# Optimization experiments

Measured on AMD Instinct MI355X. Metric: run time of the kernel, lower is better.

Reference implementation:

```python
import jax, jax.numpy as jnp
import numpy as np

B, C, H, W = 4, 512, 64, 64
CI = C // 4  # inner dim of q/k/v projections


def setup_inputs() -> dict:
    key = jax.random.key(0)
    ks = jax.random.split(key, 9)
    s = 1.0 / np.sqrt(C)
    si = 1.0 / np.sqrt(CI)
    return {
        "x": jax.random.normal(ks[0], (B, C, H, W), dtype=jnp.float32),
        "wq": jax.random.uniform(ks[1], (CI, C), jnp.float32, -s, s),
        "bq": jax.random.uniform(ks[2], (CI,), jnp.float32, -s, s),
        "wk": jax.random.uniform(ks[3], (CI, C), jnp.float32, -s, s),
        "bk": jax.random.uniform(ks[4], (CI,), jnp.float32, -s, s),
        "wv": jax.random.uniform(ks[5], (CI, C), jnp.float32, -s, s),
        "bv": jax.random.uniform(ks[6], (CI,), jnp.float32, -s, s),
        "wo": jax.random.uniform(ks[7], (C, CI), jnp.float32, -si, si),
        "bo": jax.random.uniform(ks[8], (C,), jnp.float32, -si, si),
    }


def reference(x, wq, bq, wk, bk, wv, bv, wo, bo):
    b, c, h, w = x.shape
    n = h * w
    xf = x.reshape(b, c, n)  # [B,C,N]
    # 1x1 convs == channel matmuls
    q = jnp.einsum('oc,bcn->bon', wq, xf) + bq[:, None]  # [B,CI,N]
    k = jnp.einsum('oc,bcn->bon', wk, xf) + bk[:, None]
    v = jnp.einsum('oc,bcn->bon', wv, xf) + bv[:, None]
    # energy[b,i,j] = sum_c q[b,c,i]*k[b,c,j]  (no scaling, per original)
    energy = jnp.einsum('bci,bcj->bij', q, k)  # [B,N,N]
    attn = jax.nn.softmax(energy, axis=-1)
    # out[b,c,i] = sum_j v[b,c,j] * attn[b,i,j]
    out = jnp.einsum('bcj,bij->bci', v, attn)  # [B,CI,N]
    out = jnp.einsum('oc,bcn->bon', wo, out) + bo[:, None]  # [B,C,N]
    out = out.reshape(b, c, h, w) + x
    return out
```

## Files before the change

### kernel.cpp

```cpp
#include <hip/hip_runtime.h>

#define N_TOK 4096
#define C_DIM 512
#define CI_DIM 128
#define B_DIM 4
#define KVSPLIT 4
#define KVBLK 32
#define NIT (N_TOK / KVSPLIT / KVBLK)
#define RESCALE_THR 8.0f

typedef unsigned short u16;
typedef unsigned int u32;
typedef unsigned long long u64;
typedef __attribute__((ext_vector_type(8))) short bf16x8;
typedef __attribute__((ext_vector_type(4))) float f32x4;
typedef __attribute__((ext_vector_type(8))) unsigned short u16x8;
typedef __attribute__((ext_vector_type(4))) float float4v;

typedef unsigned long long __attribute__((may_alias)) u64a;
typedef bf16x8 __attribute__((may_alias)) bf16x8a;
typedef u16x8 __attribute__((may_alias)) u16x8a;

__device__ __forceinline__ u16 f2bf(float f) {
    union { float f; u32 u; } v; v.f = f;
    u32 r = (v.u + 0x7fffu + ((v.u >> 16) & 1u)) >> 16;
    return (u16)r;
}
__device__ __forceinline__ float bf2f(u16 h) {
    union { u32 u; float f; } v; v.u = (u32)h << 16;
    return v.f;
}
__device__ __forceinline__ u32 cvt_pk_bf16(float a, float b) {
    u32 r;
    asm("v_cvt_pk_bf16_f32 %0, %1, %2" : "=v"(r) : "v"(a), "v"(b));
    return r;
}

__global__ __launch_bounds__(256) void xpose_kernel(
    const float* __restrict__ x, u16* __restrict__ xT)
{
    const int n0 = blockIdx.x * 64;
    const int c0 = blockIdx.y * 64;
    const int b  = blockIdx.z;
    __shared__ u16 Ts[64][72];
    const int t = threadIdx.x;

    const float* xb = x + (size_t)b * C_DIM * N_TOK;
    for (int idx = t; idx < 4096; idx += 256) {
        int c = idx >> 6, n = idx & 63;
        Ts[n][c] = f2bf(xb[(size_t)(c0 + c) * N_TOK + n0 + n]);
    }
    __syncthreads();
    u16* xTb = xT + (size_t)b * N_TOK * C_DIM;
    for (int idx = t; idx < 512; idx += 256) {
        int n = idx >> 3, c8 = idx & 7;
        *(u16x8*)&xTb[(size_t)(n0 + n) * C_DIM + c0 + c8 * 8] =
            *(u16x8*)&Ts[n][c8 * 8];
    }
}

__global__ __launch_bounds__(256) void wconv_kernel(
    const float* __restrict__ wq, const float* __restrict__ wk,
    const float* __restrict__ wv, const float* __restrict__ wo,
    u16* __restrict__ wqB, u16* __restrict__ wkB,
    u16* __restrict__ wvB, u16* __restrict__ woB)
{
    const int z = blockIdx.y;
    const float* src = (z == 0) ? wq : (z == 1) ? wk : (z == 2) ? wv : wo;
    u16* dst = (z == 0) ? wqB : (z == 1) ? wkB : (z == 2) ? wvB : woB;
    const int i0 = (blockIdx.x * 256 + threadIdx.x) * 8;
    float4v a = *(const float4v*)&src[i0];
    float4v b = *(const float4v*)&src[i0 + 4];
    u16x8 o;
    o[0] = f2bf(a[0]); o[1] = f2bf(a[1]); o[2] = f2bf(a[2]); o[3] = f2bf(a[3]);
    o[4] = f2bf(b[0]); o[5] = f2bf(b[1]); o[6] = f2bf(b[2]); o[7] = f2bf(b[3]);
    *(u16x8*)&dst[i0] = o;
}

__global__ __launch_bounds__(256) void qkv_gemm_kernel(
    const u16* __restrict__ xT,
    const u16* __restrict__ wqB, const u16* __restrict__ wkB,
    const u16* __restrict__ wvB,
    const float* __restrict__ bq, const float* __restrict__ bk,
    const float* __restrict__ bv,
    u16* __restrict__ qT, u16* __restrict__ kT, u16* __restrict__ vB)
{
    const int n0 = blockIdx.x * 128;
    const int b  = blockIdx.y;
    const int z  = blockIdx.z;
    const u16* wz = (z == 0) ? wqB : (z == 1) ? wkB : wvB;
    const float* bias = (z == 0) ? bq : (z == 1) ? bk : bv;

    __shared__ u16 Xs[128][72];
    __shared__ u16 Ws[128][72];

    const int t  = threadIdx.x;
    const int w  = t >> 6;
    const int l  = t & 63;
    const int lg = l >> 4;
    const int li = l & 15;
    const int cb = w * 32;

    const u16* xTb = xT + (size_t)b * N_TOK * C_DIM;

    const int srow = t >> 1;
    const int sh   = (t & 1) * 32;

    f32x4 acc[8][2];
#pragma unroll
    for (int m = 0; m < 8; ++m)
#pragma unroll
        for (int j = 0; j < 2; ++j)
#pragma unroll
            for (int r = 0; r < 4; ++r) acc[m][j][r] = 0.f;

    u16x8 xv[4], wv[4];
#pragma unroll
    for (int g = 0; g < 4; ++g) {
        xv[g] = *(const u16x8a*)&xTb[(size_t)(n0 + srow) * C_DIM + sh + g * 8];
        wv[g] = *(const u16x8a*)&wz[(size_t)srow * C_DIM + sh + g * 8];
    }

    const u16 (*A_lds)[72] = (z < 2) ? Xs : Ws;
    const u16 (*B_lds)[72] = (z < 2) ? Ws : Xs;

#pragma unroll 1
    for (int kk = 0; kk < C_DIM / 64; ++kk) {
        __syncthreads();
#pragma unroll
        for (int g = 0; g < 4; ++g) {
            *(u16x8a*)&Xs[srow][sh + g * 8] = xv[g];
            *(u16x8a*)&Ws[srow][sh + g * 8] = wv[g];
        }
        __syncthreads();

        if (kk + 1 < C_DIM / 64) {
            const int k0 = (kk + 1) * 64;
#pragma unroll
            for (int g = 0; g < 4; ++g) {
                xv[g] = *(const u16x8a*)&xTb[(size_t)(n0 + srow) * C_DIM + k0 + sh + g * 8];
                wv[g] = *(const u16x8a*)&wz[(size_t)srow * C_DIM + k0 + sh + g * 8];
            }
        }

#pragma unroll
        for (int kc = 0; kc < 2; ++kc) {
            bf16x8 af[8], bfv[2];
#pragma unroll
            for (int m = 0; m < 8; ++m)
                af[m] = *(const bf16x8a*)&A_lds[m * 16 + li][kc * 32 + lg * 8];
#pragma unroll
            for (int j = 0; j < 2; ++j)
                bfv[j] = *(const bf16x8a*)&B_lds[cb + j * 16 + li][kc * 32 + lg * 8];
            __builtin_amdgcn_s_setprio(1);
#pragma unroll
            for (int m = 0; m < 8; ++m)
#pragma unroll
                for (int j = 0; j < 2; ++j)
                    acc[m][j] = __builtin_amdgcn_mfma_f32_16x16x32_bf16(
                        af[m], bfv[j], acc[m][j], 0, 0, 0);
            __builtin_amdgcn_s_setprio(0);
        }
    }

    if (z < 2) {
        u16* dst = ((z == 0) ? qT : kT) + (size_t)b * N_TOK * CI_DIM;
#pragma unroll
        for (int j = 0; j < 2; ++j) {
            float bia = bias[cb + j * 16 + li];
#pragma unroll
            for (int m = 0; m < 8; ++m)
#pragma unroll
                for (int r = 0; r < 4; ++r)
                    dst[(size_t)(n0 + m * 16 + lg * 4 + r) * CI_DIM + cb + j * 16 + li] =
                        f2bf(acc[m][j][r] + bia);
        }
    } else {
        u16* dst = vB + (size_t)b * CI_DIM * N_TOK;
#pragma unroll
        for (int m = 0; m < 8; ++m)
#pragma unroll
            for (int r = 0; r < 4; ++r) {
                int o = m * 16 + lg * 4 + r;
                float bia = bias[o];
#pragma unroll
                for (int j = 0; j < 2; ++j)
                    dst[(size_t)o * N_TOK + n0 + cb + j * 16 + li] =
                        f2bf(acc[m][j][r] + bia);
            }
    }
}

__global__ __launch_bounds__(256) void attn_mfma_kernel(
    const u16* __restrict__ qT,
    const u16* __restrict__ kT,
    const u16* __restrict__ vB,
    u16* __restrict__ Opart,
    float* __restrict__ Mout,
    float* __restrict__ Lout)
{
    const int x   = blockIdx.x;
    const int qb  = x >> 4;
    const int b   = x & 3;
    const int kvh = (x >> 2) & 3;
    const int j_beg = kvh * (N_TOK / KVSPLIT);

    __shared__ u16 Ks[KVBLK][152];
    __shared__ u16 Vs[CI_DIM][56];
    __shared__ u16 Ps[4][32][40];

    const int t  = threadIdx.x;
    const int w  = t >> 6;
    const int l  = t & 63;
    const int lg = l >> 4;
    const int li = l & 15;
    const int qw = qb * 128 + w * 32;

    const int krow = t >> 3, kc8 = t & 7;
    const int vch  = t >> 1, vh  = t & 1;

    const u16* qTb = qT + (size_t)b * N_TOK * CI_DIM;
    const u16* kTb = kT + (size_t)b * N_TOK * CI_DIM;
    const u16* vBb = vB + (size_t)b * CI_DIM * N_TOK;

    bf16x8 qf[2][4];
#pragma unroll
    for (int qt = 0; qt < 2; ++qt)
#pragma unroll
        for (int kc = 0; kc < 4; ++kc)
            qf[qt][kc] = *(const bf16x8*)&qTb[(size_t)(qw + qt * 16 + li) * CI_DIM + kc * 32 + lg * 8];

    f32x4 Oacc[2][8];
#pragma unroll
    for (int qt = 0; qt < 2; ++qt)
#pragma unroll
        for (int ct = 0; ct < 8; ++ct)
#pragma unroll
            for (int r = 0; r < 4; ++r) Oacc[qt][ct][r] = 0.f;

    float mrun[2] = {-1e30f, -1e30f};
    float lrun[2] = {0.f, 0.f};

    u16x8 kv0, kv1, vv0, vv1;
    {
        const u16* ksrc = &kTb[(size_t)(j_beg + krow) * CI_DIM + kc8 * 16];
        kv0 = *(const u16x8a*)&ksrc[0];
        kv1 = *(const u16x8a*)&ksrc[8];
        const u16* vsrc = &vBb[(size_t)vch * N_TOK + j_beg + vh * 16];
        vv0 = *(const u16x8a*)&vsrc[0];
        vv1 = *(const u16x8a*)&vsrc[8];
    }

#pragma unroll 1
    for (int it = 0; it < NIT; ++it) {
        __syncthreads();
        *(u16x8a*)&Ks[krow][kc8 * 16]     = kv0;
        *(u16x8a*)&Ks[krow][kc8 * 16 + 8] = kv1;
        *(u16x8a*)&Vs[vch][vh * 16]       = vv0;
        *(u16x8a*)&Vs[vch][vh * 16 + 8]   = vv1;
        __syncthreads();

        if (it + 1 < NIT) {
            const int jn = j_beg + (it + 1) * KVBLK;
            const u16* ksrc = &kTb[(size_t)(jn + krow) * CI_DIM + kc8 * 16];
            kv0 = *(const u16x8a*)&ksrc[0];
            kv1 = *(const u16x8a*)&ksrc[8];
            const u16* vsrc = &vBb[(size_t)vch * N_TOK + jn + vh * 16];
            vv0 = *(const u16x8a*)&vsrc[0];
            vv1 = *(const u16x8a*)&vsrc[8];
        }

        bf16x8 ak[2][4];
#pragma unroll
        for (int jt = 0; jt < 2; ++jt)
#pragma unroll
            for (int kc = 0; kc < 4; ++kc)
                ak[jt][kc] = *(const bf16x8a*)&Ks[jt * 16 + li][kc * 32 + lg * 8];

        f32x4 sacc[2][2];
#pragma unroll
        for (int qt = 0; qt < 2; ++qt)
#pragma unroll
            for (int jt = 0; jt < 2; ++jt)
#pragma unroll
                for (int r = 0; r < 4; ++r) sacc[qt][jt][r] = 0.f;
        __builtin_amdgcn_s_setprio(1);
#pragma unroll
        for (int jt = 0; jt < 2; ++jt)
#pragma unroll
            for (int kc = 0; kc < 4; ++kc) {
                sacc[0][jt] = __builtin_amdgcn_mfma_f32_16x16x32_bf16(ak[jt][kc], qf[0][kc], sacc[0][jt], 0, 0, 0);
                sacc[1][jt] = __builtin_amdgcn_mfma_f32_16x16x32_bf16(ak[jt][kc], qf[1][kc], sacc[1][jt], 0, 0, 0);
            }
        __builtin_amdgcn_s_setprio(0);

#pragma unroll
        for (int qt = 0; qt < 2; ++qt) {
            float tl = sacc[qt][0][0];
#pragma unroll
            for (int jt = 0; jt < 2; ++jt)
#pragma unroll
                for (int r = 0; r < 4; ++r) tl = fmaxf(tl, sacc[qt][jt][r]);

            if (__any(tl > mrun[qt] + RESCALE_THR)) {
                float tmax = fmaxf(tl, __shfl_xor(tl, 16));
                tmax = fmaxf(tmax, __shfl_xor(tmax, 32));
                float mold = mrun[qt];
                float mnew = fmaxf(mold, tmax);
                float scale = __expf(mold - mnew);
                lrun[qt] *= scale;
                mrun[qt] = mnew;
#pragma unroll
                for (int r = 0; r < 4; ++r) {
                    float sc_r = __shfl(scale, lg * 4 + r);
#pragma unroll
                    for (int ct = 0; ct < 8; ++ct) Oacc[qt][ct][r] *= sc_r;
                }
            }
            float m = mrun[qt];
            float psum = 0.f;
#pragma unroll
            for (int jt = 0; jt < 2; ++jt) {
                float p0 = __expf(sacc[qt][jt][0] - m);
                float p1 = __expf(sacc[qt][jt][1] - m);
                float p2 = __expf(sacc[qt][jt][2] - m);
                float p3 = __expf(sacc[qt][jt][3] - m);
                psum += (p0 + p1) + (p2 + p3);
                u32 lo = cvt_pk_bf16(p0, p1);
                u32 hi = cvt_pk_bf16(p2, p3);
                u64 pk = (u64)lo | ((u64)hi << 32);
                *(u64a*)&Ps[w][qt * 16 + li][jt * 16 + lg * 4] = pk;
            }
            lrun[qt] += psum;
        }

        asm volatile("" ::: "memory");

        bf16x8 ap0 = *(const bf16x8a*)&Ps[w][li][lg * 8];
        bf16x8 ap1 = *(const bf16x8a*)&Ps[w][16 + li][lg * 8];
        __builtin_amdgcn_s_setprio(1);
#pragma unroll
        for (int ct = 0; ct < 8; ++ct) {
            bf16x8 bv = *(const bf16x8a*)&Vs[ct * 16 + li][lg * 8];
            Oacc[0][ct] = __builtin_amdgcn_mfma_f32_16x16x32_bf16(ap0, bv, Oacc[0][ct], 0, 0, 0);
            Oacc[1][ct] = __builtin_amdgcn_mfma_f32_16x16x32_bf16(ap1, bv, Oacc[1][ct], 0, 0, 0);
        }
        __builtin_amdgcn_s_setprio(0);
    }

#pragma unroll
    for (int qt = 0; qt < 2; ++qt) {
        lrun[qt] += __shfl_xor(lrun[qt], 16);
        lrun[qt] += __shfl_xor(lrun[qt], 32);
    }
    const size_t mlbase = ((size_t)kvh * B_DIM + b) * N_TOK + qw;
    if (lg == 0) {
#pragma unroll
        for (int qt = 0; qt < 2; ++qt) {
            Mout[mlbase + qt * 16 + li] = mrun[qt];
            Lout[mlbase + qt * 16 + li] = lrun[qt];
        }
    }
    u16* Ob = Opart + mlbase * CI_DIM;
#pragma unroll
    for (int qt = 0; qt < 2; ++qt)
#pragma unroll
        for (int ct = 0; ct < 8; ++ct)
#pragma unroll
            for (int r = 0; r < 4; ++r)
                Ob[(size_t)(qt * 16 + lg * 4 + r) * CI_DIM + ct * 16 + li] =
                    f2bf(Oacc[qt][ct][r]);
}

__global__ __launch_bounds__(256) void attn_merge_kernel(
    const u16* __restrict__ Opart, const float* __restrict__ Mout,
    const float* __restrict__ Lout, u16* __restrict__ attnoB)
{
    const int qb = blockIdx.x;
    const int b  = blockIdx.y;
    const int t  = threadIdx.x;
    const int i  = qb * 64 + (t & 63);
    const int c0 = (t >> 6) * 32;

    size_t ns[KVSPLIT];
    float cs[KVSPLIT];
    float m = -1e30f;
#pragma unroll
    for (int s = 0; s < KVSPLIT; ++s) {
        ns[s] = ((size_t)s * B_DIM + b) * N_TOK + i;
        cs[s] = Mout[ns[s]];
        m = fmaxf(m, cs[s]);
    }
    float den = 0.f;
#pragma unroll
    for (int s = 0; s < KVSPLIT; ++s) {
        cs[s] = __expf(cs[s] - m);
        den += Lout[ns[s]] * cs[s];
    }
    float inv = 1.f / den;
#pragma unroll
    for (int s = 0; s < KVSPLIT; ++s) cs[s] *= inv;

    u16* ab = attnoB + ((size_t)b * N_TOK + i) * CI_DIM;
#pragma unroll
    for (int g = 0; g < 4; ++g) {
        float acc[8];
#pragma unroll
        for (int e = 0; e < 8; ++e) acc[e] = 0.f;
#pragma unroll
        for (int s = 0; s < KVSPLIT; ++s) {
            u16x8 ov = *(const u16x8*)&Opart[ns[s] * CI_DIM + c0 + g * 8];
#pragma unroll
            for (int e = 0; e < 8; ++e) acc[e] += bf2f(ov[e]) * cs[s];
        }
        u16x8 res;
#pragma unroll
        for (int e = 0; e < 8; ++e) res[e] = f2bf(acc[e]);
        *(u16x8*)&ab[c0 + g * 8] = res;
    }
}

__global__ __launch_bounds__(256) void out_gemm_kernel(
    const u16* __restrict__ attnoB,
    const u16* __restrict__ woB,
    const float* __restrict__ bo,
    const float* __restrict__ x,
    float* __restrict__ out)
{
    const int n0 = blockIdx.x * 64;
    const int b  = blockIdx.y;
    const int t  = threadIdx.x;
    const int w  = t >> 6;
    const int l  = t & 63;
    const int lg = l >> 4;
    const int li = l & 15;
    const int co0 = w * 128;

    const u16* ab = attnoB + (size_t)b * N_TOK * CI_DIM;

    f32x4 acc[8][4];
#pragma unroll
    for (int m = 0; m < 8; ++m)
#pragma unroll
        for (int j = 0; j < 4; ++j)
#pragma unroll
            for (int r = 0; r < 4; ++r) acc[m][j][r] = 0.f;

    const u16* Abase = woB + (size_t)(co0 + li) * CI_DIM + lg * 8;
    const u16* Bbase = ab + (size_t)(n0 + li) * CI_DIM + lg * 8;

#pragma unroll
    for (int kk = 0; kk < 4; ++kk) {
        bf16x8 af[8], bfv[4];
#pragma unroll
        for (int m = 0; m < 8; ++m)
            af[m] = *(const bf16x8*)&Abase[(size_t)(m * 16) * CI_DIM + kk * 32];
#pragma unroll
        for (int j = 0; j < 4; ++j)
            bfv[j] = *(const bf16x8*)&Bbase[(size_t)(j * 16) * CI_DIM + kk * 32];
#pragma unroll
        for (int m = 0; m < 8; ++m)
#pragma unroll
            for (int j = 0; j < 4; ++j)
                acc[m][j] = __builtin_amdgcn_mfma_f32_16x16x32_bf16(
                    af[m], bfv[j], acc[m][j], 0, 0, 0);
    }

    const size_t base = (size_t)b * C_DIM * N_TOK;
#pragma unroll
    for (int m = 0; m < 8; ++m)
#pragma unroll
        for (int r = 0; r < 4; ++r) {
            int co = co0 + m * 16 + lg * 4 + r;
            float bia = bo[co];
#pragma unroll
            for (int j = 0; j < 4; ++j) {
                size_t idx = base + (size_t)co * N_TOK + n0 + j * 16 + li;
                out[idx] = acc[m][j][r] + bia + x[idx];
            }
        }
}

extern "C" void kernel_launch(void* const* d_in, const int* in_sizes, int n_in,
                              void* d_out, int out_size, void* d_ws, size_t ws_size,
                              hipStream_t stream) {
    const float* x  = (const float*)d_in[0];
    const float* wq = (const float*)d_in[1];
    const float* bq = (const float*)d_in[2];
    const float* wk = (const float*)d_in[3];
    const float* bk = (const float*)d_in[4];
    const float* wv = (const float*)d_in[5];
    const float* bv = (const float*)d_in[6];
    const float* wo = (const float*)d_in[7];
    const float* bo = (const float*)d_in[8];
    float* out = (float*)d_out;

    char* ws = (char*)d_ws;
    const size_t MB = 1024 * 1024;
    u16*   xT    = (u16*)(ws);
    u16*   Opart = (u16*)(ws);
    u16*   wqB   = (u16*)(ws + 16 * MB);
    u16*   wkB   = (u16*)(ws + 16 * MB + 128 * 1024);
    u16*   wvB   = (u16*)(ws + 16 * MB + 256 * 1024);
    u16*   woB   = (u16*)(ws + 16 * MB + 384 * 1024);
    u16*   qT    = (u16*)(ws + 16 * MB + 512 * 1024);
    u16*   kT    = (u16*)(ws + 20 * MB + 512 * 1024);
    u16*   vB    = (u16*)(ws + 24 * MB + 512 * 1024);
    float* Mout  = (float*)(ws + 28 * MB + 512 * 1024);
    float* Lout  = (float*)(ws + 28 * MB + 768 * 1024);
    u16*  attnoB = (u16*)(ws + 29 * MB);

    xpose_kernel<<<dim3(64, 8, 4), 256, 0, stream>>>(x, xT);
    wconv_kernel<<<dim3(32, 4), 256, 0, stream>>>(
        wq, wk, wv, wo, wqB, wkB, wvB, woB);
    qkv_gemm_kernel<<<dim3(32, 4, 3), 256, 0, stream>>>(
        xT, wqB, wkB, wvB, bq, bk, bv, qT, kT, vB);
    attn_mfma_kernel<<<dim3(512), 256, 0, stream>>>(
        qT, kT, vB, Opart, Mout, Lout);
    attn_merge_kernel<<<dim3(64, 4), 256, 0, stream>>>(
        Opart, Mout, Lout, attnoB);
    out_gemm_kernel<<<dim3(64, 4), 256, 0, stream>>>(
        attnoB, woB, bo, x, out);
}
```

Measured before the change: 107.1 us.

## Halve queries per wave in attention kernel to double block count

Each wave now processes 16 query rows instead of 32, so a block covers 64 queries and the grid grows from 512 to 1024 blocks, with launch bounds requesting 4 blocks per SIMD group. This cuts register use (half the accumulators and Q fragments) to raise occupancy and fill more CUs. In exchange, every K/V tile loaded into shared memory is reused by half as many queries, doubling K/V global and LDS traffic per unit of work and halving MFMA work per LDS read of K and V.

```diff
diff --git a/kernel.cpp b/kernel.cpp
--- a/kernel.cpp
+++ b/kernel.cpp
@@ -191,7 +191,7 @@
     }
 }
 
-__global__ __launch_bounds__(256) void attn_mfma_kernel(
+__global__ __launch_bounds__(256, 4) void attn_mfma_kernel(
     const u16* __restrict__ qT,
     const u16* __restrict__ kT,
     const u16* __restrict__ vB,
@@ -207,14 +207,14 @@
 
     __shared__ u16 Ks[KVBLK][152];
     __shared__ u16 Vs[CI_DIM][56];
-    __shared__ u16 Ps[4][32][40];
+    __shared__ u16 Ps[4][16][40];
 
     const int t  = threadIdx.x;
     const int w  = t >> 6;
     const int l  = t & 63;
     const int lg = l >> 4;
     const int li = l & 15;
-    const int qw = qb * 128 + w * 32;
+    const int qw = qb * 64 + w * 16;
 
     const int krow = t >> 3, kc8 = t & 7;
     const int vch  = t >> 1, vh  = t & 1;
@@ -223,23 +223,19 @@
     const u16* kTb = kT + (size_t)b * N_TOK * CI_DIM;
     const u16* vBb = vB + (size_t)b * CI_DIM * N_TOK;
 
-    bf16x8 qf[2][4];
-#pragma unroll
-    for (int qt = 0; qt < 2; ++qt)
-#pragma unroll
-        for (int kc = 0; kc < 4; ++kc)
-            qf[qt][kc] = *(const bf16x8*)&qTb[(size_t)(qw + qt * 16 + li) * CI_DIM + kc * 32 + lg * 8];
-
-    f32x4 Oacc[2][8];
-#pragma unroll
-    for (int qt = 0; qt < 2; ++qt)
-#pragma unroll
-        for (int ct = 0; ct < 8; ++ct)
-#pragma unroll
-            for (int r = 0; r < 4; ++r) Oacc[qt][ct][r] = 0.f;
-
-    float mrun[2] = {-1e30f, -1e30f};
-    float lrun[2] = {0.f, 0.f};
+    bf16x8 qf[4];
+#pragma unroll
+    for (int kc = 0; kc < 4; ++kc)
+        qf[kc] = *(const bf16x8*)&qTb[(size_t)(qw + li) * CI_DIM + kc * 32 + lg * 8];
+
+    f32x4 Oacc[8];
+#pragma unroll
+    for (int ct = 0; ct < 8; ++ct)
+#pragma unroll
+        for (int r = 0; r < 4; ++r) Oacc[ct][r] = 0.f;
+
+    float mrun = -1e30f;
+    float lrun = 0.f;
 
     u16x8 kv0, kv1, vv0, vv1;
     {
@@ -277,99 +273,84 @@
             for (int kc = 0; kc < 4; ++kc)
                 ak[jt][kc] = *(const bf16x8a*)&Ks[jt * 16 + li][kc * 32 + lg * 8];
 
-        f32x4 sacc[2][2];
-#pragma unroll
-        for (int qt = 0; qt < 2; ++qt)
+        f32x4 sacc[2];
+#pragma unroll
+        for (int jt = 0; jt < 2; ++jt)
+#pragma unroll
+            for (int r = 0; r < 4; ++r) sacc[jt][r] = 0.f;
+        __builtin_amdgcn_s_setprio(1);
+#pragma unroll
+        for (int jt = 0; jt < 2; ++jt)
+#pragma unroll
+            for (int kc = 0; kc < 4; ++kc)
+                sacc[jt] = __builtin_amdgcn_mfma_f32_16x16x32_bf16(
+                    ak[jt][kc], qf[kc], sacc[jt], 0, 0, 0);
+        __builtin_amdgcn_s_setprio(0);
+
+        {
+            float tl = sacc[0][0];
 #pragma unroll
             for (int jt = 0; jt < 2; ++jt)
 #pragma unroll
-                for (int r = 0; r < 4; ++r) sacc[qt][jt][r] = 0.f;
-        __builtin_amdgcn_s_setprio(1);
-#pragma unroll
-        for (int jt = 0; jt < 2; ++jt)
-#pragma unroll
-            for (int kc = 0; kc < 4; ++kc) {
-                sacc[0][jt] = __builtin_amdgcn_mfma_f32_16x16x32_bf16(ak[jt][kc], qf[0][kc], sacc[0][jt], 0, 0, 0);
-                sacc[1][jt] = __builtin_amdgcn_mfma_f32_16x16x32_bf16(ak[jt][kc], qf[1][kc], sacc[1][jt], 0, 0, 0);
-            }
-        __builtin_amdgcn_s_setprio(0);
-
-#pragma unroll
-        for (int qt = 0; qt < 2; ++qt) {
-            float tl = sacc[qt][0][0];
-#pragma unroll
-            for (int jt = 0; jt < 2; ++jt)
-#pragma unroll
-                for (int r = 0; r < 4; ++r) tl = fmaxf(tl, sacc[qt][jt][r]);
-
-            if (__any(tl > mrun[qt] + RESCALE_THR)) {
+                for (int r = 0; r < 4; ++r) tl = fmaxf(tl, sacc[jt][r]);
+
+            if (__any(tl > mrun + RESCALE_THR)) {
                 float tmax = fmaxf(tl, __shfl_xor(tl, 16));
                 tmax = fmaxf(tmax, __shfl_xor(tmax, 32));
-                float mold = mrun[qt];
+                float mold = mrun;
                 float mnew = fmaxf(mold, tmax);
                 float scale = __expf(mold - mnew);
-                lrun[qt] *= scale;
-                mrun[qt] = mnew;
+                lrun *= scale;
+                mrun = mnew;
 #pragma unroll
                 for (int r = 0; r < 4; ++r) {
                     float sc_r = __shfl(scale, lg * 4 + r);
 #pragma unroll
-                    for (int ct = 0; ct < 8; ++ct) Oacc[qt][ct][r] *= sc_r;
+                    for (int ct = 0; ct < 8; ++ct) Oacc[ct][r] *= sc_r;
                 }
             }
-            float m = mrun[qt];
+            float m = mrun;
             float psum = 0.f;
 #pragma unroll
             for (int jt = 0; jt < 2; ++jt) {
-                float p0 = __expf(sacc[qt][jt][0] - m);
-                float p1 = __expf(sacc[qt][jt][1] - m);
-                float p2 = __expf(sacc[qt][jt][2] - m);
-                float p3 = __expf(sacc[qt][jt][3] - m);
+                float p0 = __expf(sacc[jt][0] - m);
+                float p1 = __expf(sacc[jt][1] - m);
+                float p2 = __expf(sacc[jt][2] - m);
+                float p3 = __expf(sacc[jt][3] - m);
                 psum += (p0 + p1) + (p2 + p3);
                 u32 lo = cvt_pk_bf16(p0, p1);
                 u32 hi = cvt_pk_bf16(p2, p3);
                 u64 pk = (u64)lo | ((u64)hi << 32);
-                *(u64a*)&Ps[w][qt * 16 + li][jt * 16 + lg * 4] = pk;
+                *(u64a*)&Ps[w][li][jt * 16 + lg * 4] = pk;
             }
-            lrun[qt] += psum;
+            lrun += psum;
         }
 
         asm volatile("" ::: "memory");
 
-        bf16x8 ap0 = *(const bf16x8a*)&Ps[w][li][lg * 8];
-        bf16x8 ap1 = *(const bf16x8a*)&Ps[w][16 + li][lg * 8];
+        bf16x8 ap = *(const bf16x8a*)&Ps[w][li][lg * 8];
         __builtin_amdgcn_s_setprio(1);
 #pragma unroll
         for (int ct = 0; ct < 8; ++ct) {
             bf16x8 bv = *(const bf16x8a*)&Vs[ct * 16 + li][lg * 8];
-            Oacc[0][ct] = __builtin_amdgcn_mfma_f32_16x16x32_bf16(ap0, bv, Oacc[0][ct], 0, 0, 0);
-            Oacc[1][ct] = __builtin_amdgcn_mfma_f32_16x16x32_bf16(ap1, bv, Oacc[1][ct], 0, 0, 0);
+            Oacc[ct] = __builtin_amdgcn_mfma_f32_16x16x32_bf16(ap, bv, Oacc[ct], 0, 0, 0);
         }
         __builtin_amdgcn_s_setprio(0);
     }
 
-#pragma unroll
-    for (int qt = 0; qt < 2; ++qt) {
-        lrun[qt] += __shfl_xor(lrun[qt], 16);
-        lrun[qt] += __shfl_xor(lrun[qt], 32);
-    }
+    lrun += __shfl_xor(lrun, 16);
+    lrun += __shfl_xor(lrun, 32);
     const size_t mlbase = ((size_t)kvh * B_DIM + b) * N_TOK + qw;
     if (lg == 0) {
-#pragma unroll
-        for (int qt = 0; qt < 2; ++qt) {
-            Mout[mlbase + qt * 16 + li] = mrun[qt];
-            Lout[mlbase + qt * 16 + li] = lrun[qt];
-        }
+        Mout[mlbase + li] = mrun;
+        Lout[mlbase + li] = lrun;
     }
     u16* Ob = Opart + mlbase * CI_DIM;
 #pragma unroll
-    for (int qt = 0; qt < 2; ++qt)
-#pragma unroll
-        for (int ct = 0; ct < 8; ++ct)
-#pragma unroll
-            for (int r = 0; r < 4; ++r)
-                Ob[(size_t)(qt * 16 + lg * 4 + r) * CI_DIM + ct * 16 + li] =
-                    f2bf(Oacc[qt][ct][r]);
+    for (int ct = 0; ct < 8; ++ct)
+#pragma unroll
+        for (int r = 0; r < 4; ++r)
+            Ob[(size_t)(lg * 4 + r) * CI_DIM + ct * 16 + li] = f2bf(Oacc[ct][r]);
 }
 
 __global__ __launch_bounds__(256) void attn_merge_kernel(
@@ -515,7 +496,7 @@
         wq, wk, wv, wo, wqB, wkB, wvB, woB);
     qkv_gemm_kernel<<<dim3(32, 4, 3), 256, 0, stream>>>(
         xT, wqB, wkB, wvB, bq, bk, bv, qT, kT, vB);
-    attn_mfma_kernel<<<dim3(512), 256, 0, stream>>>(
+    attn_mfma_kernel<<<dim3(1024), 256, 0, stream>>>(
         qT, kT, vB, Opart, Mout, Lout);
     attn_merge_kernel<<<dim3(64, 4), 256, 0, stream>>>(
         Opart, Mout, Lout, attnoB);
```

After: 111.8 us. +4.3%, slower.
